# Kernel tuning notes

Measured on AMD Instinct MI355X. Metric: run time of the kernel, lower is better.

The kernel has to match this reference:

```python
import jax, jax.numpy as jnp
import numpy as np

N_NODES = 100000
N_EDGES = 1600000
D_FEAT = 64
D_OUT = 64


def setup_inputs() -> dict:
    key = jax.random.key(0)
    ks = jax.random.split(key, 8)
    return {
        "feat": jax.random.normal(ks[0], (N_NODES, D_FEAT), dtype=jnp.float32),
        "emb": jax.random.normal(ks[1], (N_NODES, D_OUT), dtype=jnp.float32),
        "W1": jax.random.normal(ks[2], (D_OUT, D_FEAT), dtype=jnp.float32) * 0.1,
        "b1": jax.random.normal(ks[3], (D_OUT,), dtype=jnp.float32) * 0.1,
        "W2": jax.random.normal(ks[4], (D_OUT, D_OUT), dtype=jnp.float32) * 0.1,
        "b2": jax.random.normal(ks[5], (D_OUT,), dtype=jnp.float32) * 0.1,
        "edge_src": jax.random.randint(ks[6], (N_EDGES,), 0, N_NODES, dtype=jnp.int32),
        "edge_dst": jax.random.randint(ks[7], (N_EDGES,), 0, N_NODES, dtype=jnp.int32),
    }


def reference(feat, emb, W1, b1, W2, b2, edge_src, edge_dst):
    # n2v: per-node neighbor embedding sum (vectorized gather + segment-sum)
    n_nodes = feat.shape[0]
    nbr_sum = jax.ops.segment_sum(emb[edge_src], edge_dst, num_segments=n_nodes)  # [N, D_OUT]
    new_emb = jax.nn.relu(feat @ W1.T + b1 + nbr_sum @ W2.T + b2)  # [N, D_OUT]
    # g2v: graph embedding = sum of node embeddings
    graph_emb = new_emb.sum(axis=0)  # [D_OUT]
    return graph_emb
```

## Files before the change

kernel.cpp:

```cpp
#include <hip/hip_runtime.h>

#define N_NODES 100000
#define N_EDGES 1600000
#define D 64
#define CAP 32
#define OVF_CAP 4096
#define N_TILES 1563
#define NR 8
#define SLICE_EDGES 2048
#define N_SLICES 782
#define R1_BLOCKS 64
#define ASTRIDE 136

#define NB2 782
#define BCAP2 2560
#define EPB 4096
#define P1_BLOCKS 391
#define CVT_BLOCKS 256

#define F2_TPB 3
#define F2_BLOCKS 521

typedef int    vint4  __attribute__((ext_vector_type(4)));
typedef short  s16x4  __attribute__((ext_vector_type(4)));
typedef short  s16x8  __attribute__((ext_vector_type(8)));
typedef float  f32x2  __attribute__((ext_vector_type(2)));
typedef float  f32x4  __attribute__((ext_vector_type(4)));
typedef __bf16 bf16x8 __attribute__((ext_vector_type(8)));

__device__ inline short f2bf(float f) {
    unsigned u = __builtin_bit_cast(unsigned, f);
    u += 0x7fffu + ((u >> 16) & 1u);
    return (short)(u >> 16);
}
__device__ inline s16x4 f2bf4(float4 v) {
    s16x4 r; r.x = f2bf(v.x); r.y = f2bf(v.y); r.z = f2bf(v.z); r.w = f2bf(v.w);
    return r;
}
__device__ inline float bf2f(short s) {
    return __builtin_bit_cast(float, ((unsigned)(unsigned short)s) << 16);
}

#define WS_SLOTS_OFF  401408
#define WS_ACC_OFF    13201408
#define WS_ACC16_OFF  13201408
#define WS_OVFC_OFF   38801408
#define WS_BCNT_OFF   38801424
#define WS_OVF_OFF    38804560
#define WS_PART_OFF   38867200
#define WS_PART2_OFF  39267328
#define WS_EMB8_OFF   39283712
#define WS_NEEDED     (WS_PART2_OFF + R1_BLOCKS * 64 * 4)
#define WS_NEEDED16   (WS_EMB8_OFF + N_NODES * D * 2)

__global__ __launch_bounds__(512) void part_kernel(
    const int* __restrict__ edge_src, const int* __restrict__ edge_dst,
    int* __restrict__ bcnt, int* __restrict__ bkt,
    int* __restrict__ ovf_cnt, int2* __restrict__ ovf,
    const float* __restrict__ emb, unsigned* __restrict__ emb8) {
    const int tid = threadIdx.x;
    if (blockIdx.x >= P1_BLOCKS) {
        const float4* e4 = (const float4*)emb;
        const unsigned t0 = (blockIdx.x - P1_BLOCKS) * 512 + tid;
        for (unsigned j = t0; j < (unsigned)(N_NODES * D / 4);
             j += CVT_BLOCKS * 512) {
            float4 v = e4[j];
            int w = 0;
            w = __builtin_amdgcn_cvt_pk_fp8_f32(v.x, v.y, w, false);
            w = __builtin_amdgcn_cvt_pk_fp8_f32(v.z, v.w, w, true);
            emb8[j] = (unsigned)w;
        }
        return;
    }

    __shared__ int stage[EPB];
    __shared__ unsigned short bid[EPB];
    __shared__ int scA[1024];
    __shared__ int scB[1024];
    __shared__ int hist[NB2];
    int* const cur   = scB;
    int* const gbase = scA;

    const int e0 = blockIdx.x * EPB;
    for (int i = tid; i < NB2; i += 512) hist[i] = 0;
    __syncthreads();

    int ss[8], dd[8];
#pragma unroll
    for (int i = 0; i < 8; ++i) {
        const int e = e0 + i * 512 + tid;
        if (e < N_EDGES) { ss[i] = edge_src[e]; dd[i] = edge_dst[e]; }
        else             { ss[i] = 0; dd[i] = -1; }
    }

#pragma unroll
    for (int i = 0; i < 8; ++i)
        if (dd[i] >= 0) atomicAdd(&hist[dd[i] >> 7], 1);
    __syncthreads();

    scA[tid]       = (tid < NB2) ? hist[tid] : 0;
    scA[tid + 512] = 0;
    if (tid + 512 < NB2) scA[tid + 512] = hist[tid + 512];
    __syncthreads();
    {
        int* sA = scA;
        int* sB = scB;
        for (int off = 1; off < 1024; off <<= 1) {
            const int i1 = tid + 512;
            const int v0 = sA[tid] + ((tid >= off) ? sA[tid - off] : 0);
            const int v1 = sA[i1] + sA[i1 - off];
            sB[tid] = v0; sB[i1] = v1;
            __syncthreads();
            int* t = sA; sA = sB; sB = t;
        }
    }
    const int tot = scA[NB2 - 1];
    for (int i = tid; i < NB2; i += 512) cur[i] = scA[i] - hist[i];
    __syncthreads();

#pragma unroll
    for (int i = 0; i < 8; ++i) {
        if (dd[i] >= 0) {
            const int b = dd[i] >> 7;
            const int pos = atomicAdd(&cur[b], 1);
            stage[pos] = (ss[i] << 7) | (dd[i] & 127);
            bid[pos] = (unsigned short)b;
        }
    }
    for (int i = tid; i < NB2; i += 512)
        gbase[i] = atomicAdd(&bcnt[i], hist[i]);
    __syncthreads();

    for (int j = tid; j < tot; j += 512) {
        const int pk = stage[j];
        const int b  = bid[j];
        const int gpos = gbase[b] + (j - (cur[b] - hist[b]));
        if (gpos < BCAP2) {
            bkt[b * BCAP2 + gpos] = pk;
        } else {
            int oj = atomicAdd(ovf_cnt, 1);
            if (oj < OVF_CAP) ovf[oj] = make_int2(pk >> 7, (b << 7) | (pk & 127));
        }
    }
}

__global__ __launch_bounds__(512) void fillgather_kernel(
    const int* __restrict__ bcnt, const int* __restrict__ bkt,
    const unsigned* __restrict__ emb8,
    int* __restrict__ ovf_cnt, int2* __restrict__ ovf,
    short* __restrict__ acc16) {
    __shared__ int lcnt[128];
    __shared__ int lslots[128 * CAP];
    const int b = blockIdx.x;
    const int tid = threadIdx.x;
    if (tid < 128) lcnt[tid] = 0;
    __syncthreads();

    int n = bcnt[b];
    if (n > BCAP2) n = BCAP2;
    for (int i = tid; i < n; i += 512) {
        const int pk = bkt[b * BCAP2 + i];
        const int dl = pk & 127;
        const int pos = atomicAdd(&lcnt[dl], 1);
        if (pos < CAP) {
            lslots[dl * CAP + pos] = pk >> 7;
        } else {
            int j = atomicAdd(ovf_cnt, 1);
            if (j < OVF_CAP) ovf[j] = make_int2(pk >> 7, (b << 7) | dl);
        }
    }
    __syncthreads();

    const int lane = tid & 63;
    const int wave = tid >> 6;
    const int q = lane >> 4;
    const int c = lane & 15;
#pragma unroll 1
    for (int t = 0; t < 16; ++t) {
        const int dl = wave * 16 + t;
        const int v = (b << 7) | dl;
        int deg = lcnt[dl];
        if (deg > CAP) deg = CAP;
        const int si = lslots[dl * CAP + (lane & (CAP - 1))];

        float4 sum = make_float4(0.f, 0.f, 0.f, 0.f);
        for (int e = 0; e < deg; e += 8) {
            const int i0 = e + q, i1 = e + 4 + q;
            const int s0 = __shfl(si, i0 & (CAP - 1));
            const int s1 = __shfl(si, i1 & (CAP - 1));
            unsigned x0 = 0u, x1 = 0u;
            if (i0 < deg) x0 = emb8[(unsigned)s0 * 16 + c];
            if (i1 < deg) x1 = emb8[(unsigned)s1 * 16 + c];
            const f32x2 a0 = __builtin_amdgcn_cvt_pk_f32_fp8((int)x0, false);
            const f32x2 a1 = __builtin_amdgcn_cvt_pk_f32_fp8((int)x0, true);
            const f32x2 b0 = __builtin_amdgcn_cvt_pk_f32_fp8((int)x1, false);
            const f32x2 b1 = __builtin_amdgcn_cvt_pk_f32_fp8((int)x1, true);
            sum.x += a0.x + b0.x;
            sum.y += a0.y + b0.y;
            sum.z += a1.x + b1.x;
            sum.w += a1.y + b1.y;
        }
#pragma unroll
        for (int off = 16; off < 64; off <<= 1) {
            sum.x += __shfl_xor(sum.x, off);
            sum.y += __shfl_xor(sum.y, off);
            sum.z += __shfl_xor(sum.z, off);
            sum.w += __shfl_xor(sum.w, off);
        }
        if (q == 0 && v < N_NODES) {
            *(s16x4*)&acc16[v * D + c * 4] = f2bf4(sum);
        }
    }
}

__global__ __launch_bounds__(64) void ovf2_kernel(
    const float* __restrict__ emb, const int* __restrict__ ovf_cnt,
    const int2* __restrict__ ovf, short* __restrict__ acc16) {
    int n = *ovf_cnt;
    if (n > OVF_CAP) n = OVF_CAP;
    const int l = threadIdx.x;
    for (int i = 0; i < n; ++i) {
        const int2 e = ovf[i];
        const float a = bf2f(acc16[e.y * D + l]) + emb[e.x * D + l];
        acc16[e.y * D + l] = f2bf(a);
    }
}

__global__ __launch_bounds__(256) void fill_kernel(
    const int* __restrict__ edge_src, const int* __restrict__ edge_dst,
    int* __restrict__ cnt, int* __restrict__ slots,
    int* __restrict__ ovf_cnt, int2* __restrict__ ovf) {
    const int r = blockIdx.x & (NR - 1);
    if (r == 7) return;
    const int slice = blockIdx.x >> 3;
    const int base_e = slice * SLICE_EDGES + threadIdx.x * 8;
    if (base_e >= N_EDGES) return;
    const vint4* s4 = (const vint4*)(edge_src + base_e);
    const vint4* d4 = (const vint4*)(edge_dst + base_e);
    vint4 a0 = __builtin_nontemporal_load(s4);
    vint4 a1 = __builtin_nontemporal_load(s4 + 1);
    vint4 b0 = __builtin_nontemporal_load(d4);
    vint4 b1 = __builtin_nontemporal_load(d4 + 1);
    int ss[8] = {a0.x, a0.y, a0.z, a0.w, a1.x, a1.y, a1.z, a1.w};
    int dd[8] = {b0.x, b0.y, b0.z, b0.w, b1.x, b1.y, b1.z, b1.w};
    int pos[8];
#pragma unroll
    for (int i = 0; i < 8; ++i) {
        pos[i] = ((dd[i] >> 14) == r) ? atomicAdd(&cnt[dd[i]], 1) : -1;
    }
#pragma unroll
    for (int i = 0; i < 8; ++i) {
        if (pos[i] >= 0 && pos[i] < CAP) slots[dd[i] * CAP + pos[i]] = ss[i];
    }
#pragma unroll
    for (int i = 0; i < 8; ++i) {
        if (pos[i] >= CAP) {
            int j = atomicAdd(ovf_cnt, 1);
            if (j < OVF_CAP) ovf[j] = make_int2(ss[i], dd[i]);
        }
    }
}

__global__ __launch_bounds__(256) void gather_kernel(
    const float* __restrict__ emb, const int* __restrict__ cnt,
    const int* __restrict__ slots, float* __restrict__ acc) {
    const int lane = threadIdx.x & 63;
    const int wave = threadIdx.x >> 6;
    const int v = blockIdx.x * 4 + wave;
    const int q  = lane >> 4;
    const int c4 = lane & 15;
    int deg = cnt[v];
    if (deg > CAP) deg = CAP;
    const int si = slots[v * CAP + (lane & (CAP - 1))];
    const float4* emb4 = (const float4*)emb;

    float4 sum = make_float4(0.f, 0.f, 0.f, 0.f);
    for (int e = 0; e < deg; e += 4) {
        const int idx = e + q;
        const int s = __shfl(si, idx & (CAP - 1));
        if (idx < deg) {
            float4 a = emb4[s * 16 + c4];
            sum.x += a.x; sum.y += a.y; sum.z += a.z; sum.w += a.w;
        }
    }
#pragma unroll
    for (int off = 16; off < 64; off <<= 1) {
        sum.x += __shfl_xor(sum.x, off);
        sum.y += __shfl_xor(sum.y, off);
        sum.z += __shfl_xor(sum.z, off);
        sum.w += __shfl_xor(sum.w, off);
    }
    if (q == 0) {
        ((float4*)acc)[v * 16 + c4] = sum;
    }
}

__global__ __launch_bounds__(256) void ovf_kernel(
    const float* __restrict__ emb, const int* __restrict__ ovf_cnt,
    const int2* __restrict__ ovf, float* __restrict__ acc) {
    int n = *ovf_cnt;
    if (n > OVF_CAP) n = OVF_CAP;
    const int lane = threadIdx.x & 63;
    const int wv = (blockIdx.x * 256 + threadIdx.x) >> 6;
    const int nwaves = (gridDim.x * 256) >> 6;
    for (int i = wv; i < n; i += nwaves) {
        int2 e = ovf[i];
        unsafeAtomicAdd(&acc[e.y * D + lane], emb[e.x * D + lane]);
    }
}

__global__ __launch_bounds__(256) void scatter_kernel(
    const float* __restrict__ emb,
    const int* __restrict__ edge_src, const int* __restrict__ edge_dst,
    float* __restrict__ acc) {
    int gid = blockIdx.x * 256 + threadIdx.x;
    int e = gid >> 6;
    int c = gid & 63;
    unsafeAtomicAdd(&acc[edge_dst[e] * D + c], emb[edge_src[e] * D + c]);
}

__global__ __launch_bounds__(256) void final_mixed2_kernel(
    const float* __restrict__ feat, const short* __restrict__ acc16,
    const float* __restrict__ W1, const float* __restrict__ b1,
    const float* __restrict__ W2, const float* __restrict__ b2,
    float* __restrict__ partials) {
    __shared__ short A_s[64 * ASTRIDE];
    __shared__ short W_s[64 * ASTRIDE];
    __shared__ float red[4][64];

    const int tid  = threadIdx.x;
    const int lane = tid & 63;
    const int wave = tid >> 6;
    const int quad = lane >> 4;
    const int col  = lane & 15;

    float bias[4];
#pragma unroll
    for (int nb = 0; nb < 4; ++nb) {
        const int o = nb * 16 + col;
        bias[nb] = b1[o] + b2[o];
    }

    {
        const float4* W1v = (const float4*)W1;
        const float4* W2v = (const float4*)W2;
#pragma unroll
        for (int i = 0; i < 4; ++i) {
            const int flat = tid + i * 256;
            const int row = flat >> 4, c4 = flat & 15;
            *(s16x4*)&W_s[row * ASTRIDE + c4 * 4]      = f2bf4(W1v[flat]);
            *(s16x4*)&W_s[row * ASTRIDE + 64 + c4 * 4] = f2bf4(W2v[flat]);
        }
    }
    __syncthreads();

    bf16x8 Bf[4][4];
#pragma unroll
    for (int nb = 0; nb < 4; ++nb)
#pragma unroll
        for (int ks = 0; ks < 4; ++ks)
            Bf[nb][ks] = __builtin_bit_cast(bf16x8,
                *(const s16x8*)&W_s[(nb * 16 + col) * ASTRIDE + ks * 32 + quad * 8]);

    float sums[4] = {0.f, 0.f, 0.f, 0.f};

#pragma unroll 1
    for (int t = 0; t < F2_TPB; ++t) {
        const int tile = blockIdx.x * F2_TPB + t;
        const int node0 = tile * 64;

        {
            const float4* fv = (const float4*)feat;
#pragma unroll
            for (int i = 0; i < 4; ++i) {
                const int flat = tid + i * 256;
                const int row = flat >> 4, c4 = flat & 15;
                const int node = node0 + row;
                float4 f = make_float4(0.f, 0.f, 0.f, 0.f);
                if (node < N_NODES) f = fv[(size_t)node * 16 + c4];
                *(s16x4*)&A_s[row * ASTRIDE + c4 * 4] = f2bf4(f);
            }
#pragma unroll
            for (int i = 0; i < 2; ++i) {
                const int flat = tid + i * 256;
                const int row = flat >> 3, c = flat & 7;
                const int node = node0 + row;
                s16x8 pk = {0, 0, 0, 0, 0, 0, 0, 0};
                if (node < N_NODES) pk = *(const s16x8*)&acc16[node * D + c * 8];
                *(s16x8*)&A_s[row * ASTRIDE + 64 + c * 8] = pk;
            }
        }
        __syncthreads();

        f32x4 C[4];
#pragma unroll
        for (int nb = 0; nb < 4; ++nb) C[nb] = (f32x4){0.f, 0.f, 0.f, 0.f};
#pragma unroll
        for (int ks = 0; ks < 4; ++ks) {
            const bf16x8 Af = __builtin_bit_cast(bf16x8,
                *(const s16x8*)&A_s[(wave * 16 + col) * ASTRIDE + ks * 32 + quad * 8]);
#pragma unroll
            for (int nb = 0; nb < 4; ++nb)
                C[nb] = __builtin_amdgcn_mfma_f32_16x16x32_bf16(Af, Bf[nb][ks],
                                                                C[nb], 0, 0, 0);
        }

#pragma unroll
        for (int nb = 0; nb < 4; ++nb) {
#pragma unroll
            for (int reg = 0; reg < 4; ++reg) {
                const int node = node0 + wave * 16 + quad * 4 + reg;
                float u = C[nb][reg] + bias[nb];
                u = (u > 0.f) ? u : 0.f;
                if (node < N_NODES) sums[nb] += u;
            }
        }
        __syncthreads();
    }

#pragma unroll
    for (int nb = 0; nb < 4; ++nb) {
        sums[nb] += __shfl_xor(sums[nb], 16);
        sums[nb] += __shfl_xor(sums[nb], 32);
        if (lane < 16) red[wave][nb * 16 + lane] = sums[nb];
    }
    __syncthreads();
    if (tid < 64) {
        partials[blockIdx.x * 64 + tid] =
            red[0][tid] + red[1][tid] + red[2][tid] + red[3][tid];
    }
}

__global__ __launch_bounds__(256) void final_kernel(
    const float* __restrict__ feat, const float* __restrict__ acc,
    const float* __restrict__ W1, const float* __restrict__ b1,
    const float* __restrict__ W2, const float* __restrict__ b2,
    float* __restrict__ partials) {
    __shared__ short A_s[64 * ASTRIDE];
    __shared__ short W_s[64 * ASTRIDE];
    __shared__ float red[4][64];

    const int tid  = threadIdx.x;
    const int lane = tid & 63;
    const int wave = tid >> 6;
    const int quad = lane >> 4;
    const int col  = lane & 15;
    const int node0 = blockIdx.x * 64;

    float bias[4];
#pragma unroll
    for (int nb = 0; nb < 4; ++nb) {
        const int o = nb * 16 + col;
        bias[nb] = b1[o] + b2[o];
    }

    {
        const float4* W1v = (const float4*)W1;
        const float4* W2v = (const float4*)W2;
#pragma unroll
        for (int i = 0; i < 4; ++i) {
            const int flat = tid + i * 256;
            const int row = flat >> 4, c4 = flat & 15;
            *(s16x4*)&W_s[row * ASTRIDE + c4 * 4]      = f2bf4(W1v[flat]);
            *(s16x4*)&W_s[row * ASTRIDE + 64 + c4 * 4] = f2bf4(W2v[flat]);
        }
    }

    {
        const float4* fv = (const float4*)feat;
        const float4* av = (const float4*)acc;
#pragma unroll
        for (int i = 0; i < 4; ++i) {
            const int flat = tid + i * 256;
            const int row = flat >> 4, c4 = flat & 15;
            const int node = node0 + row;
            float4 f = make_float4(0.f, 0.f, 0.f, 0.f);
            float4 n = make_float4(0.f, 0.f, 0.f, 0.f);
            if (node < N_NODES) {
                f = fv[(size_t)node * 16 + c4];
                n = av[(size_t)node * 16 + c4];
            }
            *(s16x4*)&A_s[row * ASTRIDE + c4 * 4]      = f2bf4(f);
            *(s16x4*)&A_s[row * ASTRIDE + 64 + c4 * 4] = f2bf4(n);
        }
    }
    __syncthreads();

    bf16x8 Bf[4][4];
#pragma unroll
    for (int nb = 0; nb < 4; ++nb)
#pragma unroll
        for (int ks = 0; ks < 4; ++ks)
            Bf[nb][ks] = __builtin_bit_cast(bf16x8,
                *(const s16x8*)&W_s[(nb * 16 + col) * ASTRIDE + ks * 32 + quad * 8]);

    f32x4 C[4];
#pragma unroll
    for (int nb = 0; nb < 4; ++nb) C[nb] = (f32x4){0.f, 0.f, 0.f, 0.f};
#pragma unroll
    for (int ks = 0; ks < 4; ++ks) {
        const bf16x8 Af = __builtin_bit_cast(bf16x8,
            *(const s16x8*)&A_s[(wave * 16 + col) * ASTRIDE + ks * 32 + quad * 8]);
#pragma unroll
        for (int nb = 0; nb < 4; ++nb)
            C[nb] = __builtin_amdgcn_mfma_f32_16x16x32_bf16(Af, Bf[nb][ks],
                                                            C[nb], 0, 0, 0);
    }

    float sums[4] = {0.f, 0.f, 0.f, 0.f};
#pragma unroll
    for (int nb = 0; nb < 4; ++nb) {
#pragma unroll
        for (int reg = 0; reg < 4; ++reg) {
            const int node = node0 + wave * 16 + quad * 4 + reg;
            float u = C[nb][reg] + bias[nb];
            u = (u > 0.f) ? u : 0.f;
            if (node < N_NODES) sums[nb] += u;
        }
        sums[nb] += __shfl_xor(sums[nb], 16);
        sums[nb] += __shfl_xor(sums[nb], 32);
        if (lane < 16) red[wave][nb * 16 + lane] = sums[nb];
    }
    __syncthreads();
    if (tid < 64) {
        partials[blockIdx.x * 64 + tid] =
            red[0][tid] + red[1][tid] + red[2][tid] + red[3][tid];
    }
}

__global__ __launch_bounds__(256) void reduce1_kernel(
    const float* __restrict__ partials, float* __restrict__ part2,
    int nrows, int rpb) {
    __shared__ float red[4][64];
    const int col = threadIdx.x & 63;
    const int seg = threadIdx.x >> 6;
    const int r0 = blockIdx.x * rpb;
    int r1 = r0 + rpb;
    if (r1 > nrows) r1 = nrows;
    float s = 0.f;
    for (int r = r0 + seg; r < r1; r += 4) s += partials[r * 64 + col];
    red[seg][col] = s;
    __syncthreads();
    if (seg == 0) {
        part2[blockIdx.x * 64 + col] =
            red[0][col] + red[1][col] + red[2][col] + red[3][col];
    }
}

__global__ __launch_bounds__(256) void reduce2_kernel(
    const float* __restrict__ part2, float* __restrict__ out) {
    __shared__ float red[4][64];
    const int col = threadIdx.x & 63;
    const int seg = threadIdx.x >> 6;
    float s = 0.f;
    for (int r = seg; r < R1_BLOCKS; r += 4) s += part2[r * 64 + col];
    red[seg][col] = s;
    __syncthreads();
    if (seg == 0) {
        out[col] = red[0][col] + red[1][col] + red[2][col] + red[3][col];
    }
}

extern "C" void kernel_launch(void* const* d_in, const int* in_sizes, int n_in,
                              void* d_out, int out_size, void* d_ws, size_t ws_size,
                              hipStream_t stream) {
    const float* feat = (const float*)d_in[0];
    const float* emb  = (const float*)d_in[1];
    const float* W1   = (const float*)d_in[2];
    const float* b1   = (const float*)d_in[3];
    const float* W2   = (const float*)d_in[4];
    const float* b2   = (const float*)d_in[5];
    const int* edge_src = (const int*)d_in[6];
    const int* edge_dst = (const int*)d_in[7];
    float* out = (float*)d_out;
    char* ws = (char*)d_ws;

    if (ws_size >= (size_t)WS_NEEDED16) {
        int*      bkt      = (int*)ws;
        short*    acc16    = (short*)(ws + WS_ACC16_OFF);
        int*      ovf_cnt  = (int*)(ws + WS_OVFC_OFF);
        int*      bcnt     = (int*)(ws + WS_BCNT_OFF);
        int2*     ovf      = (int2*)(ws + WS_OVF_OFF);
        float*    partials = (float*)(ws + WS_PART_OFF);
        float*    part2    = (float*)(ws + WS_PART2_OFF);
        unsigned* emb8     = (unsigned*)(ws + WS_EMB8_OFF);

        (void)hipMemsetAsync(ovf_cnt, 0, 16 + NB2 * sizeof(int), stream);

        part_kernel<<<P1_BLOCKS + CVT_BLOCKS, 512, 0, stream>>>(
            edge_src, edge_dst, bcnt, bkt, ovf_cnt, ovf, emb, emb8);
        fillgather_kernel<<<NB2, 512, 0, stream>>>(bcnt, bkt, emb8,
                                                   ovf_cnt, ovf, acc16);
        ovf2_kernel<<<1, 64, 0, stream>>>(emb, ovf_cnt, ovf, acc16);

        final_mixed2_kernel<<<F2_BLOCKS, 256, 0, stream>>>(feat, acc16, W1, b1,
                                                           W2, b2, partials);
        reduce1_kernel<<<R1_BLOCKS, 256, 0, stream>>>(partials, part2,
                                                      F2_BLOCKS, 9);
        reduce2_kernel<<<1, 256, 0, stream>>>(part2, out);
    } else if (ws_size >= (size_t)WS_NEEDED) {
        int*   cnt      = (int*)ws;
        int*   slots    = (int*)(ws + WS_SLOTS_OFF);
        float* acc      = (float*)(ws + WS_ACC_OFF);
        int*   ovf_cnt  = (int*)(ws + WS_OVFC_OFF);
        int2*  ovf      = (int2*)(ws + WS_OVF_OFF);
        float* partials = (float*)(ws + WS_PART_OFF);
        float* part2    = (float*)(ws + WS_PART2_OFF);

        (void)hipMemsetAsync(cnt, 0, N_NODES * sizeof(int), stream);
        (void)hipMemsetAsync(ovf_cnt, 0, sizeof(int), stream);

        fill_kernel<<<NR * N_SLICES, 256, 0, stream>>>(edge_src, edge_dst,
                                                       cnt, slots, ovf_cnt, ovf);
        gather_kernel<<<N_NODES / 4, 256, 0, stream>>>(emb, cnt, slots, acc);
        ovf_kernel<<<16, 256, 0, stream>>>(emb, ovf_cnt, ovf, acc);

        final_kernel<<<N_TILES, 256, 0, stream>>>(feat, acc, W1, b1, W2, b2,
                                                  partials);
        reduce1_kernel<<<R1_BLOCKS, 256, 0, stream>>>(partials, part2,
                                                      N_TILES, 25);
        reduce2_kernel<<<1, 256, 0, stream>>>(part2, out);
    } else {
        float* acc = (float*)ws;
        (void)hipMemsetAsync(acc, 0, (size_t)N_NODES * D * sizeof(float), stream);
        scatter_kernel<<<(N_EDGES * 64) / 256, 256, 0, stream>>>(emb, edge_src,
                                                                 edge_dst, acc);
        float* partials = (float*)(ws + (size_t)N_NODES * D * sizeof(float));
        float* part2    = partials + (size_t)N_TILES * 64;
        final_kernel<<<N_TILES, 256, 0, stream>>>(feat, acc, W1, b1, W2, b2,
                                                  partials);
        reduce1_kernel<<<R1_BLOCKS, 256, 0, stream>>>(partials, part2,
                                                      N_TILES, 25);
        reduce2_kernel<<<1, 256, 0, stream>>>(part2, out);
    }
}
```

Baseline: 184.3 us.

## Fold overflow handling into fillgather and reduce partials via atomics into output

Overflow edges are now collected per block in shared memory and applied by wave 0 of each fillgather block, which removes the separate single-block ovf2 kernel. Overflow that spills to the global list is filtered by bucket inside each block. The final kernel atomically adds its block partials straight into the output, which part_kernel zeroes first, so the two reduce kernels go away. Together this drops three launches from the chain. The cost is an extra serial tail in each fillgather block, a nondeterministic float summation order in the output, and overflow contributions now read from the fp8 copy of emb instead of fp32.

```diff
diff --git a/kernel.cpp b/kernel.cpp
--- a/kernel.cpp
+++ b/kernel.cpp
@@ -5,6 +5,7 @@
 #define D 64
 #define CAP 32
 #define OVF_CAP 4096
+#define LOVF_CAP 256
 #define N_TILES 1563
 #define NR 8
 #define SLICE_EDGES 2048
@@ -57,11 +58,14 @@
     const int* __restrict__ edge_src, const int* __restrict__ edge_dst,
     int* __restrict__ bcnt, int* __restrict__ bkt,
     int* __restrict__ ovf_cnt, int2* __restrict__ ovf,
-    const float* __restrict__ emb, unsigned* __restrict__ emb8) {
+    const float* __restrict__ emb, unsigned* __restrict__ emb8,
+    float* __restrict__ out) {
     const int tid = threadIdx.x;
     if (blockIdx.x >= P1_BLOCKS) {
+        const int rid = blockIdx.x - P1_BLOCKS;
+        if (rid == 0 && tid < 64) out[tid] = 0.f;
         const float4* e4 = (const float4*)emb;
-        const unsigned t0 = (blockIdx.x - P1_BLOCKS) * 512 + tid;
+        const unsigned t0 = rid * 512 + tid;
         for (unsigned j = t0; j < (unsigned)(N_NODES * D / 4);
              j += CVT_BLOCKS * 512) {
             float4 v = e4[j];
@@ -151,9 +155,12 @@
     short* __restrict__ acc16) {
     __shared__ int lcnt[128];
     __shared__ int lslots[128 * CAP];
+    __shared__ int lovf[LOVF_CAP];
+    __shared__ int lovf_cnt;
     const int b = blockIdx.x;
     const int tid = threadIdx.x;
     if (tid < 128) lcnt[tid] = 0;
+    if (tid == 0) lovf_cnt = 0;
     __syncthreads();
 
     int n = bcnt[b];
@@ -165,8 +172,13 @@
         if (pos < CAP) {
             lslots[dl * CAP + pos] = pk >> 7;
         } else {
-            int j = atomicAdd(ovf_cnt, 1);
-            if (j < OVF_CAP) ovf[j] = make_int2(pk >> 7, (b << 7) | dl);
+            int j = atomicAdd(&lovf_cnt, 1);
+            if (j < LOVF_CAP) {
+                lovf[j] = pk;
+            } else {
+                int g = atomicAdd(ovf_cnt, 1);
+                if (g < OVF_CAP) ovf[g] = make_int2(pk >> 7, (b << 7) | dl);
+            }
         }
     }
     __syncthreads();
@@ -211,18 +223,45 @@
             *(s16x4*)&acc16[v * D + c * 4] = f2bf4(sum);
         }
     }
-}
-
-__global__ __launch_bounds__(64) void ovf2_kernel(
-    const float* __restrict__ emb, const int* __restrict__ ovf_cnt,
-    const int2* __restrict__ ovf, short* __restrict__ acc16) {
-    int n = *ovf_cnt;
-    if (n > OVF_CAP) n = OVF_CAP;
-    const int l = threadIdx.x;
-    for (int i = 0; i < n; ++i) {
-        const int2 e = ovf[i];
-        const float a = bf2f(acc16[e.y * D + l]) + emb[e.x * D + l];
-        acc16[e.y * D + l] = f2bf(a);
+    __syncthreads();
+
+    if (wave == 0) {
+        int nl = lovf_cnt;
+        if (nl > LOVF_CAP) nl = LOVF_CAP;
+        for (int i = 0; i < nl; ++i) {
+            const int pk = lovf[i];
+            const int v = (b << 7) | (pk & 127);
+            if (lane < 16) {
+                const unsigned x = emb8[(unsigned)(pk >> 7) * 16 + lane];
+                const f32x2 lo = __builtin_amdgcn_cvt_pk_f32_fp8((int)x, false);
+                const f32x2 hi = __builtin_amdgcn_cvt_pk_f32_fp8((int)x, true);
+                s16x4 cu = *(s16x4*)&acc16[v * D + lane * 4];
+                s16x4 r;
+                r.x = f2bf(bf2f(cu.x) + lo.x);
+                r.y = f2bf(bf2f(cu.y) + lo.y);
+                r.z = f2bf(bf2f(cu.z) + hi.x);
+                r.w = f2bf(bf2f(cu.w) + hi.y);
+                *(s16x4*)&acc16[v * D + lane * 4] = r;
+            }
+        }
+        int ng = *ovf_cnt;
+        if (ng > OVF_CAP) ng = OVF_CAP;
+        for (int i = 0; i < ng; ++i) {
+            const int2 e = ovf[i];
+            if ((e.y >> 7) != b) continue;
+            if (lane < 16) {
+                const unsigned x = emb8[(unsigned)e.x * 16 + lane];
+                const f32x2 lo = __builtin_amdgcn_cvt_pk_f32_fp8((int)x, false);
+                const f32x2 hi = __builtin_amdgcn_cvt_pk_f32_fp8((int)x, true);
+                s16x4 cu = *(s16x4*)&acc16[e.y * D + lane * 4];
+                s16x4 r;
+                r.x = f2bf(bf2f(cu.x) + lo.x);
+                r.y = f2bf(bf2f(cu.y) + lo.y);
+                r.z = f2bf(bf2f(cu.z) + hi.x);
+                r.w = f2bf(bf2f(cu.w) + hi.y);
+                *(s16x4*)&acc16[e.y * D + lane * 4] = r;
+            }
+        }
     }
 }
 
@@ -323,7 +362,7 @@
     const float* __restrict__ feat, const short* __restrict__ acc16,
     const float* __restrict__ W1, const float* __restrict__ b1,
     const float* __restrict__ W2, const float* __restrict__ b2,
-    float* __restrict__ partials) {
+    float* __restrict__ out) {
     __shared__ short A_s[64 * ASTRIDE];
     __shared__ short W_s[64 * ASTRIDE];
     __shared__ float red[4][64];
@@ -426,8 +465,8 @@
     }
     __syncthreads();
     if (tid < 64) {
-        partials[blockIdx.x * 64 + tid] =
-            red[0][tid] + red[1][tid] + red[2][tid] + red[3][tid];
+        unsafeAtomicAdd(&out[tid],
+            red[0][tid] + red[1][tid] + red[2][tid] + red[3][tid]);
     }
 }
 
@@ -581,23 +620,16 @@
         int*      ovf_cnt  = (int*)(ws + WS_OVFC_OFF);
         int*      bcnt     = (int*)(ws + WS_BCNT_OFF);
         int2*     ovf      = (int2*)(ws + WS_OVF_OFF);
-        float*    partials = (float*)(ws + WS_PART_OFF);
-        float*    part2    = (float*)(ws + WS_PART2_OFF);
         unsigned* emb8     = (unsigned*)(ws + WS_EMB8_OFF);
 
         (void)hipMemsetAsync(ovf_cnt, 0, 16 + NB2 * sizeof(int), stream);
 
         part_kernel<<<P1_BLOCKS + CVT_BLOCKS, 512, 0, stream>>>(
-            edge_src, edge_dst, bcnt, bkt, ovf_cnt, ovf, emb, emb8);
+            edge_src, edge_dst, bcnt, bkt, ovf_cnt, ovf, emb, emb8, out);
         fillgather_kernel<<<NB2, 512, 0, stream>>>(bcnt, bkt, emb8,
                                                    ovf_cnt, ovf, acc16);
-        ovf2_kernel<<<1, 64, 0, stream>>>(emb, ovf_cnt, ovf, acc16);
-
         final_mixed2_kernel<<<F2_BLOCKS, 256, 0, stream>>>(feat, acc16, W1, b1,
-                                                           W2, b2, partials);
-        reduce1_kernel<<<R1_BLOCKS, 256, 0, stream>>>(partials, part2,
-                                                      F2_BLOCKS, 9);
-        reduce2_kernel<<<1, 256, 0, stream>>>(part2, out);
+                                                           W2, b2, out);
     } else if (ws_size >= (size_t)WS_NEEDED) {
         int*   cnt      = (int*)ws;
         int*   slots    = (int*)(ws + WS_SLOTS_OFF);
```

Result: faster. 170.6 us, median of 2 (-7.5%).
